# Optimization experiments

Hardware: AMD Instinct MI355X
Metric: run time of the kernel (lower is better)

Reference implementation:

```python
import jax, jax.numpy as jnp
import numpy as np

N_NODES = 131072
B_GRAPHS = 16
L_MAX = 8192  # nodes per graph (equal partition -> static dense shape)
CHANNELS = 512
HEAD_CH = 128  # head_channels, heads fixed to 1


def _to_dense_batch(x, batch, num_graphs, max_nodes):
    # Mirrors torch_geometric.utils.to_dense_batch for a sorted batch vector.
    n = x.shape[0]
    counts = jnp.zeros((num_graphs,), jnp.int32).at[batch].add(1)
    offsets = jnp.concatenate([jnp.zeros((1,), jnp.int32), jnp.cumsum(counts)[:-1]])
    pos = jnp.arange(n, dtype=jnp.int32) - offsets[batch]
    dense = jnp.zeros((num_graphs, max_nodes, x.shape[1]), x.dtype).at[batch, pos].set(x)
    mask = jnp.zeros((num_graphs, max_nodes), bool).at[batch, pos].set(True)
    return dense, mask


def setup_inputs() -> dict:
    key = jax.random.key(0)
    kx, kq, kk, kv = jax.random.split(key, 4)
    x = jax.random.normal(kx, (N_NODES, CHANNELS), jnp.float32)
    scale = 1.0 / np.sqrt(CHANNELS)
    Wq = jax.random.normal(kq, (HEAD_CH, CHANNELS), jnp.float32) * scale
    Wk = jax.random.normal(kk, (HEAD_CH, CHANNELS), jnp.float32) * scale
    Wv = jax.random.normal(kv, (HEAD_CH, CHANNELS), jnp.float32) * scale
    # sorted batch vector: equal-size graphs so L_MAX is static
    batch = (jnp.arange(N_NODES, dtype=jnp.int32) // L_MAX).astype(jnp.int32)
    return {"x": x, "Wq": Wq, "Wk": Wk, "Wv": Wv, "batch": batch,
            "num_graphs": B_GRAPHS, "max_nodes": L_MAX}


def reference(x, Wq, Wk, Wv, batch, num_graphs, max_nodes):
    B, L, H, M = num_graphs, max_nodes, 1, Wq.shape[0]
    xd, mask = _to_dense_batch(x, batch, B, L)  # [B, L, C]; padded rows are zero
    qs = (xd @ Wq.T).reshape(B, L, H, M)
    ks = (xd @ Wk.T).reshape(B, L, H, M)
    vs = (xd @ Wv.T).reshape(B, L, H, M)
    # GLOBAL (scalar) Frobenius norm, as in torch.norm(t, p=2)
    qs = qs / jnp.linalg.norm(qs)
    ks = ks / jnp.linalg.norm(ks)
    n_const = qs.shape[0]  # source uses qs.shape[0] (= batch size) here
    # linear attention: K^T V first, then Q (K^T V)
    kvs = jnp.einsum('blhm,blhd->bhmd', ks, vs)
    attention_num = jnp.einsum('bnhm,bhmd->bnhd', qs, kvs) + n_const * vs
    ks_sum = ks.sum(axis=1)  # [B, H, M]
    attention_normalizer = jnp.einsum('bnhm,bhm->bnh', qs, ks_sum)[..., None] + n_const
    attn_output = attention_num / attention_normalizer  # [B, L, H, M]
    return attn_output
```

## Files before the change

### kernel.cpp

```cpp
#include <hip/hip_runtime.h>
#include <hip/hip_bf16.h>

typedef __bf16 bf16;
typedef __bf16 bf16x4 __attribute__((ext_vector_type(4)));
typedef __bf16 bf16x8 __attribute__((ext_vector_type(8)));
typedef float f32x4 __attribute__((ext_vector_type(4)));

#define N_NODES 131072
#define CH      512
#define HD      128
#define LMAX    8192
#define NG      16

typedef __attribute__((address_space(3))) unsigned int lds_u32;
typedef __attribute__((address_space(1))) const unsigned int g_u32;

__device__ __forceinline__ void gload16(const void* gp, void* lp) {
    __builtin_amdgcn_global_load_lds((g_u32*)gp, (lds_u32*)lp, 16, 0, 0);
}

__global__ __launch_bounds__(256, 1) void k0_prep(
    const float* __restrict__ Wq, const float* __restrict__ Wk,
    const float* __restrict__ Wv, bf16* __restrict__ wsW)
{
    int t = blockIdx.x * 256 + threadIdx.x;
    int c = t / 3072;
    int r = t % 3072;
    int j = r >> 3, g = r & 7;
    const float* Wrow = (j < 128) ? (Wq + (size_t)j * CH)
                       : (j < 256) ? (Wk + (size_t)(j - 128) * CH)
                                   : (Wv + (size_t)(j - 256) * CH);
    int col0 = ((g ^ (j & 7)) << 3);
    const float* src = Wrow + c * 64 + col0;
    float4 f0 = *(const float4*)src;
    float4 f1 = *(const float4*)(src + 4);
    bf16x8 o;
    o[0] = (bf16)f0.x; o[1] = (bf16)f0.y; o[2] = (bf16)f0.z; o[3] = (bf16)f0.w;
    o[4] = (bf16)f1.x; o[5] = (bf16)f1.y; o[6] = (bf16)f1.z; o[7] = (bf16)f1.w;
    *(bf16x8*)(wsW + (size_t)t * 8) = o;
}

__global__ __launch_bounds__(512, 1) void k1_proj(
    const float* __restrict__ x, const bf16* __restrict__ wsW,
    bf16* __restrict__ qo, bf16* __restrict__ ko, bf16* __restrict__ vo,
    float* __restrict__ sumsq)
{
    __shared__ bf16 As[2][128][72];
    __shared__ bf16 Bs[2][24576];
    __shared__ float rq[8], rk[8];

    const int tid = threadIdx.x;
    const int lane = tid & 63;
    const int w = tid >> 6;
    const int wr = w >> 2, wc = w & 3;
    const int lr = lane & 15, lh = lane >> 4;
    const int n0 = blockIdx.x * 128;
    const int ar = tid >> 4, ac4 = tid & 15;

    f32x4 acc[4][6];
    #pragma unroll
    for (int mi = 0; mi < 4; mi++)
        #pragma unroll
        for (int ni = 0; ni < 6; ni++)
            acc[mi][ni] = (f32x4){0.f, 0.f, 0.f, 0.f};

    float4 aregs[4];

    {
        const char* wb = (const char*)wsW + w * 1024 + lane * 16;
        char* db = (char*)(&Bs[0][0]) + w * 1024;
        #pragma unroll
        for (int i = 0; i < 6; i++) gload16(wb + i * 8192, db + i * 8192);
        #pragma unroll
        for (int i = 0; i < 4; i++)
            aregs[i] = *(const float4*)(x + (size_t)(n0 + ar + i * 32) * CH + ac4 * 4);
        #pragma unroll
        for (int i = 0; i < 4; i++) {
            bf16x4 t; t[0] = (bf16)aregs[i].x; t[1] = (bf16)aregs[i].y;
                      t[2] = (bf16)aregs[i].z; t[3] = (bf16)aregs[i].w;
            *(bf16x4*)&As[0][ar + i * 32][ac4 * 4] = t;
        }
        __syncthreads();
    }

    for (int c = 0; c < 8; c++) {
        const int cur = c & 1, nxt = cur ^ 1;
        if (c < 7) {
            const char* wb = (const char*)wsW + (size_t)(c + 1) * 49152 + w * 1024 + lane * 16;
            char* db = (char*)(&Bs[nxt][0]) + w * 1024;
            #pragma unroll
            for (int i = 0; i < 6; i++) gload16(wb + i * 8192, db + i * 8192);
            #pragma unroll
            for (int i = 0; i < 4; i++)
                aregs[i] = *(const float4*)(x + (size_t)(n0 + ar + i * 32) * CH + (c + 1) * 64 + ac4 * 4);
        }
        #pragma unroll
        for (int kk = 0; kk < 64; kk += 32) {
            bf16x8 a[4], b[6];
            #pragma unroll
            for (int mi = 0; mi < 4; mi++)
                a[mi] = *(const bf16x8*)&As[cur][wr * 64 + mi * 16 + lr][kk + lh * 8];
            #pragma unroll
            for (int ni = 0; ni < 6; ni++) {
                int j = wc * 96 + ni * 16 + lr;
                int colx = (kk + lh * 8) ^ ((lr & 7) << 3);
                b[ni] = *(const bf16x8*)&Bs[cur][j * 64 + colx];
            }
            #pragma unroll
            for (int mi = 0; mi < 4; mi++)
                #pragma unroll
                for (int ni = 0; ni < 6; ni++)
                    acc[mi][ni] = __builtin_amdgcn_mfma_f32_16x16x32_bf16(
                        a[mi], b[ni], acc[mi][ni], 0, 0, 0);
        }
        if (c < 7) {
            #pragma unroll
            for (int i = 0; i < 4; i++) {
                bf16x4 t; t[0] = (bf16)aregs[i].x; t[1] = (bf16)aregs[i].y;
                          t[2] = (bf16)aregs[i].z; t[3] = (bf16)aregs[i].w;
                *(bf16x4*)&As[nxt][ar + i * 32][ac4 * 4] = t;
            }
        }
        __syncthreads();
    }

    float sq = 0.f, sk = 0.f;
    #pragma unroll
    for (int mi = 0; mi < 4; mi++) {
        #pragma unroll
        for (int ni = 0; ni < 6; ni++) {
            int col = wc * 96 + ni * 16 + lr;
            int arr = col >> 7, cc = col & 127;
            bf16* dst = (arr == 0) ? qo : (arr == 1) ? ko : vo;
            #pragma unroll
            for (int r = 0; r < 4; r++) {
                int row = n0 + wr * 64 + mi * 16 + lh * 4 + r;
                float val = acc[mi][ni][r];
                dst[(size_t)row * HD + cc] = (bf16)val;
                if (arr == 0) sq += val * val;
                else if (arr == 1) sk += val * val;
            }
        }
    }
    #pragma unroll
    for (int off = 32; off > 0; off >>= 1) {
        sq += __shfl_down(sq, off);
        sk += __shfl_down(sk, off);
    }
    if (lane == 0) { rq[w] = sq; rk[w] = sk; }
    __syncthreads();
    if (tid == 0) {
        float a = 0.f, b = 0.f;
        #pragma unroll
        for (int i = 0; i < 8; i++) { a += rq[i]; b += rk[i]; }
        atomicAdd(&sumsq[0], a);
        atomicAdd(&sumsq[1], b);
    }
}

__global__ __launch_bounds__(512, 1) void k2_kv(
    const bf16* __restrict__ ko, const bf16* __restrict__ vo,
    float* __restrict__ part_kv, float* __restrict__ part_ks)
{
    __shared__ __align__(16) char smem[16640];
    bf16 (*kt)[130] = (bf16(*)[130])smem;
    bf16 (*vt)[130] = (bf16(*)[130])(smem + 8320);
    float* scr = (float*)smem;

    const int tid = threadIdx.x, lane = tid & 63, w = tid >> 6;
    const int wr = w >> 2, wc = w & 3;
    const int lr = lane & 15, lh = lane >> 4;
    const int b = blockIdx.x >> 4, cch = blockIdx.x & 15;
    const size_t l0 = (size_t)b * LMAX + (size_t)cch * 512;
    const int sr = tid >> 4, sc = tid & 15;

    f32x4 acc[4][2];
    #pragma unroll
    for (int mi = 0; mi < 4; mi++)
        #pragma unroll
        for (int ni = 0; ni < 2; ni++)
            acc[mi][ni] = (f32x4){0.f, 0.f, 0.f, 0.f};
    float ks8[8] = {};

    uint4 kk4 = *(const uint4*)&ko[(l0 + sr) * HD + sc * 8];
    uint4 vv4 = *(const uint4*)&vo[(l0 + sr) * HD + sc * 8];

    for (int lt = 0; lt < 512; lt += 32) {
        __syncthreads();
        #pragma unroll
        for (int j2 = 0; j2 < 4; j2++) {
            *(unsigned int*)&kt[sr][sc * 8 + j2 * 2] = ((const unsigned int*)&kk4)[j2];
            *(unsigned int*)&vt[sr][sc * 8 + j2 * 2] = ((const unsigned int*)&vv4)[j2];
        }
        #pragma unroll
        for (int j = 0; j < 8; j++) ks8[j] += (float)((const bf16*)&kk4)[j];
        __syncthreads();
        if (lt + 32 < 512) {
            kk4 = *(const uint4*)&ko[(l0 + lt + 32 + sr) * HD + sc * 8];
            vv4 = *(const uint4*)&vo[(l0 + lt + 32 + sr) * HD + sc * 8];
        }
        bf16x8 a[4], bb[2];
        #pragma unroll
        for (int mi = 0; mi < 4; mi++) {
            int m = wr * 64 + mi * 16 + lr;
            #pragma unroll
            for (int j = 0; j < 8; j++) a[mi][j] = kt[lh * 8 + j][m];
        }
        #pragma unroll
        for (int ni = 0; ni < 2; ni++) {
            int d = wc * 32 + ni * 16 + lr;
            #pragma unroll
            for (int j = 0; j < 8; j++) bb[ni][j] = vt[lh * 8 + j][d];
        }
        #pragma unroll
        for (int mi = 0; mi < 4; mi++)
            #pragma unroll
            for (int ni = 0; ni < 2; ni++)
                acc[mi][ni] = __builtin_amdgcn_mfma_f32_16x16x32_bf16(
                    a[mi], bb[ni], acc[mi][ni], 0, 0, 0);
    }

    __syncthreads();
    #pragma unroll
    for (int j = 0; j < 8; j++) scr[tid * 8 + j] = ks8[j];
    __syncthreads();
    if (tid < 128) {
        float s = 0.f;
        #pragma unroll
        for (int g = 0; g < 32; g++)
            s += scr[((g << 4) | (tid >> 3)) * 8 + (tid & 7)];
        part_ks[blockIdx.x * HD + tid] = s;
    }

    float* dst = part_kv + (size_t)blockIdx.x * 16384;
    #pragma unroll
    for (int mi = 0; mi < 4; mi++)
        #pragma unroll
        for (int ni = 0; ni < 2; ni++)
            #pragma unroll
            for (int r = 0; r < 4; r++) {
                int m = wr * 64 + mi * 16 + lh * 4 + r;
                int d = wc * 32 + ni * 16 + lr;
                dst[m * HD + d] = acc[mi][ni][r];
            }
}

__global__ __launch_bounds__(256, 1) void k2b_reduce(
    const float* __restrict__ part_kv, const float* __restrict__ part_ks,
    const float* __restrict__ sumsq,
    bf16* __restrict__ kvsT, float* __restrict__ ks_sum_s)
{
    const int b = blockIdx.x >> 3, ms = blockIdx.x & 7, tid = threadIdx.x;
    const float s_qk = rsqrtf(sumsq[0]) * rsqrtf(sumsq[1]);

    #pragma unroll
    for (int i = 0; i < 8; i++) {
        int idx = i * 256 + tid;
        int m = ms * 16 + (idx >> 7), d = idx & 127;
        float s = 0.f;
        #pragma unroll
        for (int c = 0; c < 16; c++)
            s += part_kv[((size_t)(b * 16 + c) << 14) + (m << 7) + d];
        kvsT[((size_t)b << 14) + (d << 7) + m] = (bf16)(s * s_qk);
    }
    if (ms == 0 && tid < 128) {
        float s = 0.f;
        #pragma unroll
        for (int c = 0; c < 16; c++)
            s += part_ks[(b * 16 + c) * HD + tid];
        ks_sum_s[b * HD + tid] = s * s_qk;
    }
}

__global__ __launch_bounds__(256, 1) void k3_out(
    const bf16* __restrict__ qo, const bf16* __restrict__ vo,
    const bf16* __restrict__ kvsT, const float* __restrict__ ks_sum_s,
    float* __restrict__ out)
{
    __shared__ bf16 qs[128][136];
    __shared__ bf16 vsh[128][136];
    __shared__ bf16 kv[128][136];
    __shared__ float kss[128];
    __shared__ float denom[128];
    const int tid = threadIdx.x, lane = tid & 63, w = tid >> 6;
    const int lr = lane & 15, lh = lane >> 4;
    const int n0 = blockIdx.x * 128;
    const int b = n0 >> 13;

    #pragma unroll
    for (int i = 0; i < 8; i++) {
        int idx = tid + i * 256;
        int r = idx >> 4, c8 = idx & 15;
        *(bf16x8*)&qs[r][c8 * 8]  = *(const bf16x8*)&qo[(size_t)(n0 + r) * HD + c8 * 8];
        *(bf16x8*)&vsh[r][c8 * 8] = *(const bf16x8*)&vo[(size_t)(n0 + r) * HD + c8 * 8];
        *(bf16x8*)&kv[r][c8 * 8]  = *(const bf16x8*)&kvsT[(size_t)b * 16384 + (size_t)idx * 8];
    }
    if (tid < 128) kss[tid] = ks_sum_s[b * HD + tid];
    __syncthreads();

    if (tid < 128) {
        float s = 0.f;
        #pragma unroll 8
        for (int m = 0; m < HD; m++) s += (float)qs[tid][m] * kss[m];
        denom[tid] = s + 16.0f;
    }

    f32x4 acc[2][8];
    #pragma unroll
    for (int mi = 0; mi < 2; mi++)
        #pragma unroll
        for (int ni = 0; ni < 8; ni++)
            acc[mi][ni] = (f32x4){0.f, 0.f, 0.f, 0.f};

    #pragma unroll
    for (int k0 = 0; k0 < HD; k0 += 32) {
        bf16x8 a[2], bb[8];
        #pragma unroll
        for (int mi = 0; mi < 2; mi++)
            a[mi] = *(const bf16x8*)&qs[w * 32 + mi * 16 + lr][k0 + lh * 8];
        #pragma unroll
        for (int ni = 0; ni < 8; ni++)
            bb[ni] = *(const bf16x8*)&kv[ni * 16 + lr][k0 + lh * 8];
        #pragma unroll
        for (int mi = 0; mi < 2; mi++)
            #pragma unroll
            for (int ni = 0; ni < 8; ni++)
                acc[mi][ni] = __builtin_amdgcn_mfma_f32_16x16x32_bf16(
                    a[mi], bb[ni], acc[mi][ni], 0, 0, 0);
    }
    __syncthreads();

    #pragma unroll
    for (int mi = 0; mi < 2; mi++) {
        #pragma unroll
        for (int ni = 0; ni < 8; ni++) {
            int col = ni * 16 + lr;
            #pragma unroll
            for (int r = 0; r < 4; r++) {
                int row = w * 32 + mi * 16 + lh * 4 + r;
                float vv = (float)vsh[row][col];
                out[(size_t)(n0 + row) * HD + col] =
                    (acc[mi][ni][r] + 16.0f * vv) / denom[row];
            }
        }
    }
}

extern "C" void kernel_launch(void* const* d_in, const int* in_sizes, int n_in,
                              void* d_out, int out_size, void* d_ws, size_t ws_size,
                              hipStream_t stream)
{
    const float* x  = (const float*)d_in[0];
    const float* Wq = (const float*)d_in[1];
    const float* Wk = (const float*)d_in[2];
    const float* Wv = (const float*)d_in[3];

    char* ws = (char*)d_ws;
    const size_t Q_OFF   = 0;
    const size_t K_OFF   = 33554432;
    const size_t V_OFF   = 67108864;
    const size_t PKV_OFF = 100663296;
    const size_t PKS_OFF = 117440512;
    const size_t KVS_OFF = 117571584;
    const size_t KSS_OFF = 118095872;
    const size_t SSQ_OFF = 118104064;
    const size_t NEED    = 118104072;
    if (ws_size < NEED) return;

    bf16*  qo      = (bf16*)(ws + Q_OFF);
    bf16*  ko      = (bf16*)(ws + K_OFF);
    bf16*  vo      = (bf16*)(ws + V_OFF);
    float* part_kv = (float*)(ws + PKV_OFF);
    float* part_ks = (float*)(ws + PKS_OFF);
    bf16*  kvsT    = (bf16*)(ws + KVS_OFF);
    float* ks_sum  = (float*)(ws + KSS_OFF);
    float* sumsq   = (float*)(ws + SSQ_OFF);
    bf16*  wsW     = (bf16*)(ws + PKV_OFF);

    hipMemsetAsync(sumsq, 0, 8, stream);
    k0_prep<<<dim3(96), dim3(256), 0, stream>>>(Wq, Wk, Wv, wsW);
    k1_proj<<<dim3(N_NODES / 128), dim3(512), 0, stream>>>(x, wsW, qo, ko, vo, sumsq);
    k2_kv<<<dim3(256), dim3(512), 0, stream>>>(ko, vo, part_kv, part_ks);
    k2b_reduce<<<dim3(128), dim3(256), 0, stream>>>(part_kv, part_ks, sumsq, kvsT, ks_sum);
    k3_out<<<dim3(N_NODES / 128), dim3(256), 0, stream>>>(qo, vo, kvsT, ks_sum, (float*)d_out);
}
```

Baseline: 177.2 us.

## Halve projection K-tile to raise occupancy and read kvsT directly from global

The projection GEMM now uses a 32-wide K chunk instead of 64, which halves LDS use for the A and B tiles and doubles the number of pipeline steps. The weight swizzle in the prep kernel is changed to match. Launch bounds are raised so several blocks can share a CU. In the output kernel the kv tile is no longer staged in LDS; MFMA B operands are loaded straight from global, which cuts LDS so two blocks fit per CU. The trade-offs are more barriers per K step, possible register pressure under the tighter launch bounds, and repeated global reads of kvsT through cache.

```diff
diff --git a/kernel.cpp b/kernel.cpp
--- a/kernel.cpp
+++ b/kernel.cpp
@@ -24,29 +24,28 @@
     const float* __restrict__ Wv, bf16* __restrict__ wsW)
 {
     int t = blockIdx.x * 256 + threadIdx.x;
-    int c = t / 3072;
-    int r = t % 3072;
-    int j = r >> 3, g = r & 7;
+    int c = t / 1536;
+    int r = t % 1536;
+    int j = r >> 2, g = r & 3;
     const float* Wrow = (j < 128) ? (Wq + (size_t)j * CH)
                        : (j < 256) ? (Wk + (size_t)(j - 128) * CH)
                                    : (Wv + (size_t)(j - 256) * CH);
-    int col0 = ((g ^ (j & 7)) << 3);
-    const float* src = Wrow + c * 64 + col0;
-    float4 f0 = *(const float4*)src;
-    float4 f1 = *(const float4*)(src + 4);
+    int col0 = c * 32 + ((g ^ ((j >> 1) & 3)) << 3);
+    float4 f0 = *(const float4*)(Wrow + col0);
+    float4 f1 = *(const float4*)(Wrow + col0 + 4);
     bf16x8 o;
     o[0] = (bf16)f0.x; o[1] = (bf16)f0.y; o[2] = (bf16)f0.z; o[3] = (bf16)f0.w;
     o[4] = (bf16)f1.x; o[5] = (bf16)f1.y; o[6] = (bf16)f1.z; o[7] = (bf16)f1.w;
     *(bf16x8*)(wsW + (size_t)t * 8) = o;
 }
 
-__global__ __launch_bounds__(512, 1) void k1_proj(
+__global__ __launch_bounds__(512, 4) void k1_proj(
     const float* __restrict__ x, const bf16* __restrict__ wsW,
     bf16* __restrict__ qo, bf16* __restrict__ ko, bf16* __restrict__ vo,
     float* __restrict__ sumsq)
 {
-    __shared__ bf16 As[2][128][72];
-    __shared__ bf16 Bs[2][24576];
+    __shared__ bf16 As[2][128][40];
+    __shared__ bf16 Bs[2][12288];
     __shared__ float rq[8], rk[8];
 
     const int tid = threadIdx.x;
@@ -55,7 +54,7 @@
     const int wr = w >> 2, wc = w & 3;
     const int lr = lane & 15, lh = lane >> 4;
     const int n0 = blockIdx.x * 128;
-    const int ar = tid >> 4, ac4 = tid & 15;
+    const int ar = tid >> 2, ac = tid & 3;
 
     f32x4 acc[4][6];
     #pragma unroll
@@ -64,62 +63,52 @@
         for (int ni = 0; ni < 6; ni++)
             acc[mi][ni] = (f32x4){0.f, 0.f, 0.f, 0.f};
 
-    float4 aregs[4];
+    float4 areg0, areg1;
 
     {
         const char* wb = (const char*)wsW + w * 1024 + lane * 16;
         char* db = (char*)(&Bs[0][0]) + w * 1024;
         #pragma unroll
-        for (int i = 0; i < 6; i++) gload16(wb + i * 8192, db + i * 8192);
-        #pragma unroll
-        for (int i = 0; i < 4; i++)
-            aregs[i] = *(const float4*)(x + (size_t)(n0 + ar + i * 32) * CH + ac4 * 4);
-        #pragma unroll
-        for (int i = 0; i < 4; i++) {
-            bf16x4 t; t[0] = (bf16)aregs[i].x; t[1] = (bf16)aregs[i].y;
-                      t[2] = (bf16)aregs[i].z; t[3] = (bf16)aregs[i].w;
-            *(bf16x4*)&As[0][ar + i * 32][ac4 * 4] = t;
-        }
+        for (int i = 0; i < 3; i++) gload16(wb + i * 8192, db + i * 8192);
+        areg0 = *(const float4*)(x + (size_t)(n0 + ar) * CH + ac * 8);
+        areg1 = *(const float4*)(x + (size_t)(n0 + ar) * CH + ac * 8 + 4);
+        bf16x8 t;
+        t[0] = (bf16)areg0.x; t[1] = (bf16)areg0.y; t[2] = (bf16)areg0.z; t[3] = (bf16)areg0.w;
+        t[4] = (bf16)areg1.x; t[5] = (bf16)areg1.y; t[6] = (bf16)areg1.z; t[7] = (bf16)areg1.w;
+        *(bf16x8*)&As[0][ar][ac * 8] = t;
         __syncthreads();
     }
 
-    for (int c = 0; c < 8; c++) {
+    for (int c = 0; c < 16; c++) {
         const int cur = c & 1, nxt = cur ^ 1;
-        if (c < 7) {
-            const char* wb = (const char*)wsW + (size_t)(c + 1) * 49152 + w * 1024 + lane * 16;
+        if (c < 15) {
+            const char* wb = (const char*)wsW + (size_t)(c + 1) * 24576 + w * 1024 + lane * 16;
             char* db = (char*)(&Bs[nxt][0]) + w * 1024;
             #pragma unroll
-            for (int i = 0; i < 6; i++) gload16(wb + i * 8192, db + i * 8192);
-            #pragma unroll
-            for (int i = 0; i < 4; i++)
-                aregs[i] = *(const float4*)(x + (size_t)(n0 + ar + i * 32) * CH + (c + 1) * 64 + ac4 * 4);
-        }
-        #pragma unroll
-        for (int kk = 0; kk < 64; kk += 32) {
-            bf16x8 a[4], b[6];
-            #pragma unroll
-            for (int mi = 0; mi < 4; mi++)
-                a[mi] = *(const bf16x8*)&As[cur][wr * 64 + mi * 16 + lr][kk + lh * 8];
+            for (int i = 0; i < 3; i++) gload16(wb + i * 8192, db + i * 8192);
+            areg0 = *(const float4*)(x + (size_t)(n0 + ar) * CH + (c + 1) * 32 + ac * 8);
+            areg1 = *(const float4*)(x + (size_t)(n0 + ar) * CH + (c + 1) * 32 + ac * 8 + 4);
+        }
+        bf16x8 af[4];
+        #pragma unroll
+        for (int mi = 0; mi < 4; mi++)
+            af[mi] = *(const bf16x8*)&As[cur][wr * 64 + mi * 16 + lr][lh * 8];
+        #pragma unroll
+        for (int mi = 0; mi < 4; mi++) {
             #pragma unroll
             for (int ni = 0; ni < 6; ni++) {
                 int j = wc * 96 + ni * 16 + lr;
-                int colx = (kk + lh * 8) ^ ((lr & 7) << 3);
-                b[ni] = *(const bf16x8*)&Bs[cur][j * 64 + colx];
+                int g = lh ^ ((j >> 1) & 3);
+                bf16x8 bf_ = *(const bf16x8*)&Bs[cur][j * 32 + (g << 3)];
+                acc[mi][ni] = __builtin_amdgcn_mfma_f32_16x16x32_bf16(
+                    af[mi], bf_, acc[mi][ni], 0, 0, 0);
             }
-            #pragma unroll
-            for (int mi = 0; mi < 4; mi++)
-                #pragma unroll
-                for (int ni = 0; ni < 6; ni++)
-                    acc[mi][ni] = __builtin_amdgcn_mfma_f32_16x16x32_bf16(
-                        a[mi], b[ni], acc[mi][ni], 0, 0, 0);
-        }
-        if (c < 7) {
-            #pragma unroll
-            for (int i = 0; i < 4; i++) {
-                bf16x4 t; t[0] = (bf16)aregs[i].x; t[1] = (bf16)aregs[i].y;
-                          t[2] = (bf16)aregs[i].z; t[3] = (bf16)aregs[i].w;
-                *(bf16x4*)&As[nxt][ar + i * 32][ac4 * 4] = t;
-            }
+        }
+        if (c < 15) {
+            bf16x8 t;
+            t[0] = (bf16)areg0.x; t[1] = (bf16)areg0.y; t[2] = (bf16)areg0.z; t[3] = (bf16)areg0.w;
+            t[4] = (bf16)areg1.x; t[5] = (bf16)areg1.y; t[6] = (bf16)areg1.z; t[7] = (bf16)areg1.w;
+            *(bf16x8*)&As[nxt][ar][ac * 8] = t;
         }
         __syncthreads();
     }
@@ -272,14 +261,13 @@
     }
 }
 
-__global__ __launch_bounds__(256, 1) void k3_out(
+__global__ __launch_bounds__(256, 2) void k3_out(
     const bf16* __restrict__ qo, const bf16* __restrict__ vo,
     const bf16* __restrict__ kvsT, const float* __restrict__ ks_sum_s,
     float* __restrict__ out)
 {
     __shared__ bf16 qs[128][136];
     __shared__ bf16 vsh[128][136];
-    __shared__ bf16 kv[128][136];
     __shared__ float kss[128];
     __shared__ float denom[128];
     const int tid = threadIdx.x, lane = tid & 63, w = tid >> 6;
@@ -293,7 +281,6 @@
         int r = idx >> 4, c8 = idx & 15;
         *(bf16x8*)&qs[r][c8 * 8]  = *(const bf16x8*)&qo[(size_t)(n0 + r) * HD + c8 * 8];
         *(bf16x8*)&vsh[r][c8 * 8] = *(const bf16x8*)&vo[(size_t)(n0 + r) * HD + c8 * 8];
-        *(bf16x8*)&kv[r][c8 * 8]  = *(const bf16x8*)&kvsT[(size_t)b * 16384 + (size_t)idx * 8];
     }
     if (tid < 128) kss[tid] = ks_sum_s[b * HD + tid];
     __syncthreads();
@@ -320,7 +307,7 @@
             a[mi] = *(const bf16x8*)&qs[w * 32 + mi * 16 + lr][k0 + lh * 8];
         #pragma unroll
         for (int ni = 0; ni < 8; ni++)
-            bb[ni] = *(const bf16x8*)&kv[ni * 16 + lr][k0 + lh * 8];
+            bb[ni] = *(const bf16x8*)&kvsT[(size_t)b * 16384 + (size_t)(ni * 16 + lr) * HD + k0 + lh * 8];
         #pragma unroll
         for (int mi = 0; mi < 2; mi++)
             #pragma unroll
```

After: 353.6 us. +99.6%, slower.
